# Performance work log

Measured on AMD Instinct MI355X. Metric: run time of the kernel, lower is better.

The kernel has to match this reference:

```python
import jax, jax.numpy as jnp
import numpy as np

N = 50000   # nodes
E = 800000  # edges
F = 256     # feature dim (in = hidden = out)
L = 3       # number_layers


def _arma_conv(x, src, dst, w, Wi, Wr, b):
    # GCN normalization without self loops (PyG ARMAConv default)
    deg = jax.ops.segment_sum(w, dst, num_segments=N)                 # [N]
    dinv = jnp.where(deg > 0, jax.lax.rsqrt(deg), 0.0)
    norm = dinv[src] * w * dinv[dst]                                   # [E]
    h = x @ Wi                                                         # [N, F]
    agg = jax.ops.segment_sum(norm[:, None] * h[src], dst, num_segments=N)  # [N, F]
    # root dropout is inactive in eval mode
    return jax.nn.relu(agg + x @ Wr + b)


def setup_inputs() -> dict:
    key = jax.random.key(0)
    ks = jax.random.split(key, 6)
    x = jax.random.normal(ks[0], (N, F), jnp.float32)
    edge_index = jax.random.randint(ks[1], (2, E), 0, N, jnp.int32)
    edge_attr = jax.random.uniform(ks[2], (E,), jnp.float32)
    s = 1.0 / np.sqrt(F)
    W_init = jax.random.normal(ks[3], (L, F, F), jnp.float32) * s
    W_root = jax.random.normal(ks[4], (L, F, F), jnp.float32) * s
    bias = jnp.zeros((L, F), jnp.float32)
    return dict(x=x, edge_index=edge_index, edge_attr=edge_attr,
                W_init=W_init, W_root=W_root, bias=bias)


def reference(x, edge_index, edge_attr, W_init, W_root, bias):
    src, dst = edge_index[0], edge_index[1]
    for i in range(L):  # fixed small layer count
        x = _arma_conv(x, src, dst, edge_attr, W_init[i], W_root[i], bias[i])
        # outer functional.relu is a no-op after the conv's internal ReLU;
        # dropout is inactive in eval mode.
    return x
```

## Files before the change

kernel.cpp:

```cpp
#include <hip/hip_runtime.h>
#include <hip/hip_bf16.h>

#define N_NODES 50000
#define N_EDGES 800000
#define FDIM 256
#define N_LAYERS 3
#define NB_SCAN ((N_NODES + 255) / 256)

typedef __attribute__((ext_vector_type(8))) short bf16x8;
typedef __attribute__((ext_vector_type(4))) float f32x4;

__device__ inline unsigned short f2bf(float f) {
  unsigned int u = __float_as_uint(f);
  unsigned int r = u + 0x7FFFu + ((u >> 16) & 1u);
  return (unsigned short)(r >> 16);
}
__device__ inline float bf2f(unsigned short s) {
  return __uint_as_float(((unsigned int)s) << 16);
}
__device__ inline void split2(float f, unsigned short& h, unsigned short& l) {
  h = f2bf(f);
  l = f2bf(f - bf2f(h));
}

#define GLOAD16(g, l) __builtin_amdgcn_global_load_lds( \
    (const __attribute__((address_space(1))) void*)(g), \
    (__attribute__((address_space(3))) void*)(l), 16, 0, 0)


__global__ void deg_count_kernel(const int* __restrict__ dst,
                                 const float* __restrict__ w,
                                 float* __restrict__ deg,
                                 int* __restrict__ cnt, int E) {
  int e = blockIdx.x * blockDim.x + threadIdx.x;
  if (e < E) {
    int d = dst[e];
    atomicAdd(&deg[d], w[e]);
    atomicAdd(&cnt[d], 1);
  }
}

__global__ void dinv_kernel(const float* __restrict__ deg,
                            float* __restrict__ dinv, int n) {
  int i = blockIdx.x * blockDim.x + threadIdx.x;
  if (i < n) {
    float d = deg[i];
    dinv[i] = (d > 0.f) ? (1.f / sqrtf(d)) : 0.f;
  }
}

__global__ __launch_bounds__(256)
void blocksum_kernel(const int* __restrict__ cnt, int* __restrict__ bsum, int n) {
  int b = blockIdx.x;
  int t = threadIdx.x;
  int i = b * 256 + t;
  int v = (i < n) ? cnt[i] : 0;
  #pragma unroll
  for (int d = 1; d < 64; d <<= 1) v += __shfl_xor(v, d, 64);
  __shared__ int ws[4];
  if ((t & 63) == 0) ws[t >> 6] = v;
  __syncthreads();
  if (t == 0) bsum[b] = ws[0] + ws[1] + ws[2] + ws[3];
}

__global__ __launch_bounds__(256)
void scanb_kernel(const int* __restrict__ bsum, int* __restrict__ bpre,
                  int* __restrict__ offs_end) {
  int t = threadIdx.x;
  int lane = t & 63, wid = t >> 6;
  int v = (t < NB_SCAN) ? bsum[t] : 0;
  int incl = v;
  #pragma unroll
  for (int d = 1; d < 64; d <<= 1) {
    int tmp = __shfl_up(incl, d, 64);
    if (lane >= d) incl += tmp;
  }
  __shared__ int wsum[4];
  if (lane == 63) wsum[wid] = incl;
  __syncthreads();
  if (t == 0) {
    int s = 0;
    #pragma unroll
    for (int k = 0; k < 4; ++k) { int tt = wsum[k]; wsum[k] = s; s += tt; }
  }
  __syncthreads();
  int excl = incl - v + wsum[wid];
  if (t < NB_SCAN) bpre[t] = excl;
  if (t == NB_SCAN - 1) *offs_end = excl + v;
}

__global__ __launch_bounds__(256)
void offs_kernel(const int* __restrict__ cnt, const int* __restrict__ bpre,
                 int* __restrict__ offs, int* __restrict__ cursor, int n) {
  int b = blockIdx.x;
  int t = threadIdx.x;
  int lane = t & 63, wid = t >> 6;
  int i = b * 256 + t;
  int v = (i < n) ? cnt[i] : 0;
  int incl = v;
  #pragma unroll
  for (int d = 1; d < 64; d <<= 1) {
    int tmp = __shfl_up(incl, d, 64);
    if (lane >= d) incl += tmp;
  }
  __shared__ int wsum[4];
  if (lane == 63) wsum[wid] = incl;
  __syncthreads();
  if (t == 0) {
    int s = 0;
    #pragma unroll
    for (int k = 0; k < 4; ++k) { int tt = wsum[k]; wsum[k] = s; s += tt; }
  }
  __syncthreads();
  int excl = incl - v + wsum[wid] + bpre[b];
  if (i < n) { offs[i] = excl; cursor[i] = excl; }
}

__global__ void scatter_kernel(const int* __restrict__ src,
                               const int* __restrict__ dst,
                               const float* __restrict__ w,
                               const float* __restrict__ dinv,
                               int* __restrict__ cursor,
                               int* __restrict__ src_s,
                               float* __restrict__ norm_s, int E) {
  int e = blockIdx.x * blockDim.x + threadIdx.x;
  if (e < E) {
    int s = src[e], d = dst[e];
    int pos = atomicAdd(&cursor[d], 1);
    src_s[pos] = s;
    norm_s[pos] = dinv[s] * w[e] * dinv[d];
  }
}

__global__ void split_kernel(const float* __restrict__ x,
                             unsigned short* __restrict__ xhi,
                             unsigned short* __restrict__ xlo, int n4) {
  int i = blockIdx.x * blockDim.x + threadIdx.x;
  if (i < n4) {
    float4 v = reinterpret_cast<const float4*>(x)[i];
    ushort4 h, l;
    split2(v.x, h.x, l.x);
    split2(v.y, h.y, l.y);
    split2(v.z, h.z, l.z);
    split2(v.w, h.w, l.w);
    reinterpret_cast<ushort4*>(xhi)[i] = h;
    reinterpret_cast<ushort4*>(xlo)[i] = l;
  }
}

__global__ __launch_bounds__(256)
void wsplit_kernel(const float* __restrict__ Wi_a,
                   const float* __restrict__ Wr_a,
                   unsigned short* __restrict__ wthi,
                   unsigned short* __restrict__ wtlo) {
  __shared__ float tile[32][33];
  int m6 = blockIdx.x >> 6;
  int tid = blockIdx.x & 63;
  int tk = (tid >> 3) * 32;
  int tn = (tid & 7) * 32;
  int layer = m6 >> 1;
  const float* W = ((m6 & 1) ? Wr_a : Wi_a) + (size_t)layer * FDIM * FDIM;
  int t = threadIdx.x;
  int lr = t >> 3;
  int lc = (t & 7) * 4;
  float4 v = *reinterpret_cast<const float4*>(W + (size_t)(tk + lr) * FDIM + tn + lc);
  tile[lr][lc + 0] = v.x; tile[lr][lc + 1] = v.y;
  tile[lr][lc + 2] = v.z; tile[lr][lc + 3] = v.w;
  __syncthreads();
  ushort4 h, l;
  split2(tile[lc + 0][lr], h.x, l.x);
  split2(tile[lc + 1][lr], h.y, l.y);
  split2(tile[lc + 2][lr], h.z, l.z);
  split2(tile[lc + 3][lr], h.w, l.w);
  size_t o = ((size_t)m6 * FDIM + tn + lr) * FDIM + tk + lc;
  *reinterpret_cast<ushort4*>(wthi + o) = h;
  *reinterpret_cast<ushort4*>(wtlo + o) = l;
}


__global__ __launch_bounds__(256)
void agg_kernel(const unsigned short* __restrict__ xh,
                const float* __restrict__ norm_s,
                const int* __restrict__ src_s,
                const int* __restrict__ offs,
                unsigned short* __restrict__ agh,
                unsigned short* __restrict__ agl, int n) {
  int node = blockIdx.x * 4 + (threadIdx.x >> 6);
  if (node >= n) return;
  int lane = threadIdx.x & 63;
  int beg = offs[node];
  int end = offs[node + 1];
  float a0 = 0.f, a1 = 0.f, a2 = 0.f, a3 = 0.f;
  int j = beg;
  for (; j + 4 <= end; j += 4) {
    int s0 = src_s[j], s1 = src_s[j + 1], s2 = src_s[j + 2], s3 = src_s[j + 3];
    float w0 = norm_s[j], w1 = norm_s[j + 1], w2 = norm_s[j + 2], w3 = norm_s[j + 3];
    ushort4 v0 = *reinterpret_cast<const ushort4*>(xh + (size_t)s0 * FDIM + lane * 4);
    ushort4 v1 = *reinterpret_cast<const ushort4*>(xh + (size_t)s1 * FDIM + lane * 4);
    ushort4 v2 = *reinterpret_cast<const ushort4*>(xh + (size_t)s2 * FDIM + lane * 4);
    ushort4 v3 = *reinterpret_cast<const ushort4*>(xh + (size_t)s3 * FDIM + lane * 4);
    a0 += w0 * bf2f(v0.x) + w1 * bf2f(v1.x) + w2 * bf2f(v2.x) + w3 * bf2f(v3.x);
    a1 += w0 * bf2f(v0.y) + w1 * bf2f(v1.y) + w2 * bf2f(v2.y) + w3 * bf2f(v3.y);
    a2 += w0 * bf2f(v0.z) + w1 * bf2f(v1.z) + w2 * bf2f(v2.z) + w3 * bf2f(v3.z);
    a3 += w0 * bf2f(v0.w) + w1 * bf2f(v1.w) + w2 * bf2f(v2.w) + w3 * bf2f(v3.w);
  }
  for (; j < end; ++j) {
    int s = src_s[j];
    float wv = norm_s[j];
    ushort4 v = *reinterpret_cast<const ushort4*>(xh + (size_t)s * FDIM + lane * 4);
    a0 += wv * bf2f(v.x); a1 += wv * bf2f(v.y);
    a2 += wv * bf2f(v.z); a3 += wv * bf2f(v.w);
  }
  ushort4 hh, ll;
  split2(a0, hh.x, ll.x);
  split2(a1, hh.y, ll.y);
  split2(a2, hh.z, ll.z);
  split2(a3, hh.w, ll.w);
  size_t base = (size_t)node * FDIM + lane * 4;
  *reinterpret_cast<ushort4*>(agh + base) = hh;
  *reinterpret_cast<ushort4*>(agl + base) = ll;
}


#define STAGE_TILE(TI, GPTR, ROWB, CLAMP, K0)                                     \
  {                                                                               \
    int s0_ = t;                                                                  \
    int rr_ = s0_ >> 2;                                                           \
    int sl_ = (s0_ & 3) ^ ((rr_ >> 1) & 3);                                       \
    int r2_ = (ROWB) + rr_; if (CLAMP && r2_ >= M) r2_ = M - 1;                   \
    GLOAD16((GPTR) + (size_t)r2_ * FDIM + (K0) + sl_ * 8,                         \
            smem + (TI) * 8192 + s0_ * 16);                                       \
    int s1_ = t + 256;                                                            \
    rr_ = s1_ >> 2;                                                               \
    sl_ = (s1_ & 3) ^ ((rr_ >> 1) & 3);                                           \
    r2_ = (ROWB) + rr_; if (CLAMP && r2_ >= M) r2_ = M - 1;                       \
    GLOAD16((GPTR) + (size_t)r2_ * FDIM + (K0) + sl_ * 8,                         \
            smem + (TI) * 8192 + s1_ * 16);                                       \
  }

#define STAGE_ALL(K0)                      \
  STAGE_TILE(0, agh, rowBase, 1, K0);      \
  STAGE_TILE(1, agl, rowBase, 1, K0);      \
  STAGE_TILE(2, xh, rowBase, 1, K0);       \
  STAGE_TILE(3, xl, rowBase, 1, K0);       \
  STAGE_TILE(4, wih, nBase, 0, K0);        \
  STAGE_TILE(5, wil, nBase, 0, K0);        \
  STAGE_TILE(6, wrh, nBase, 0, K0);        \
  STAGE_TILE(7, wrl, nBase, 0, K0);

__global__ __launch_bounds__(256, 2)
void gemm_dual_kernel(const unsigned short* __restrict__ agh,
                      const unsigned short* __restrict__ agl,
                      const unsigned short* __restrict__ xh,
                      const unsigned short* __restrict__ xl,
                      const unsigned short* __restrict__ wih,
                      const unsigned short* __restrict__ wil,
                      const unsigned short* __restrict__ wrh,
                      const unsigned short* __restrict__ wrl,
                      const float* __restrict__ bias,
                      unsigned short* __restrict__ oh,
                      unsigned short* __restrict__ ol,
                      float* __restrict__ ofinal,
                      int writeFinal, int M) {
  __shared__ __align__(16) unsigned char smem[65536];
  const int t = threadIdx.x;
  const int lane = t & 63;
  const int w = t >> 6;
  const int bid = blockIdx.x;
  const int rowBase = (bid >> 1) * 128;
  const int nBase = (bid & 1) * 128;

  const int wm = (w >> 1) * 64;
  const int wn = (w & 1) * 64;

  f32x4 acc[4][4];
  #pragma unroll
  for (int i = 0; i < 4; ++i)
    #pragma unroll
    for (int j = 0; j < 4; ++j)
      acc[i][j] = (f32x4)(0.f);

  STAGE_ALL(0);

  for (int s = 0; s < 8; ++s) {
    __syncthreads();

    const int q = lane >> 4;
    bf16x8 fah[4], fal[4], fxh[4], fxl[4];
    bf16x8 bih[4], bil[4], brh[4], brl[4];
    #pragma unroll
    for (int i = 0; i < 4; ++i) {
      int R = wm + i * 16 + (lane & 15);
      int offA = R * 64 + ((q ^ ((R >> 1) & 3)) * 16);
      fah[i] = *reinterpret_cast<const bf16x8*>(smem + offA);
      fal[i] = *reinterpret_cast<const bf16x8*>(smem + 8192 + offA);
      fxh[i] = *reinterpret_cast<const bf16x8*>(smem + 16384 + offA);
      fxl[i] = *reinterpret_cast<const bf16x8*>(smem + 24576 + offA);
      int Rb = wn + i * 16 + (lane & 15);
      int offB = Rb * 64 + ((q ^ ((Rb >> 1) & 3)) * 16);
      bih[i] = *reinterpret_cast<const bf16x8*>(smem + 32768 + offB);
      bil[i] = *reinterpret_cast<const bf16x8*>(smem + 40960 + offB);
      brh[i] = *reinterpret_cast<const bf16x8*>(smem + 49152 + offB);
      brl[i] = *reinterpret_cast<const bf16x8*>(smem + 57344 + offB);
    }
    asm volatile("s_waitcnt lgkmcnt(0)" ::: "memory");
    __builtin_amdgcn_sched_barrier(0);
    __builtin_amdgcn_s_barrier();
    __builtin_amdgcn_sched_barrier(0);

    if (s < 7) {
      int k1 = (s + 1) * 32;
      STAGE_ALL(k1);
    }

    #pragma unroll
    for (int j = 0; j < 4; ++j) {
      #pragma unroll
      for (int i = 0; i < 4; ++i) {
        acc[i][j] = __builtin_amdgcn_mfma_f32_16x16x32_bf16(fal[i], bih[j], acc[i][j], 0, 0, 0);
        acc[i][j] = __builtin_amdgcn_mfma_f32_16x16x32_bf16(fah[i], bil[j], acc[i][j], 0, 0, 0);
        acc[i][j] = __builtin_amdgcn_mfma_f32_16x16x32_bf16(fah[i], bih[j], acc[i][j], 0, 0, 0);
        acc[i][j] = __builtin_amdgcn_mfma_f32_16x16x32_bf16(fxl[i], brh[j], acc[i][j], 0, 0, 0);
        acc[i][j] = __builtin_amdgcn_mfma_f32_16x16x32_bf16(fxh[i], brl[j], acc[i][j], 0, 0, 0);
        acc[i][j] = __builtin_amdgcn_mfma_f32_16x16x32_bf16(fxh[i], brh[j], acc[i][j], 0, 0, 0);
      }
    }
  }

  const int cr = lane & 15;
  const int r4 = (lane >> 4) * 4;
  #pragma unroll
  for (int i = 0; i < 4; ++i)
    #pragma unroll
    for (int j = 0; j < 4; ++j) {
      int col = nBase + wn + j * 16 + cr;
      float badd = bias[col];
      #pragma unroll
      for (int e = 0; e < 4; ++e) {
        int row = rowBase + wm + i * 16 + r4 + e;
        if (row < M) {
          float val = fmaxf(acc[i][j][e] + badd, 0.f);
          size_t o = (size_t)row * FDIM + col;
          if (writeFinal) {
            ofinal[o] = val;
          } else {
            unsigned short hh, ll;
            split2(val, hh, ll);
            oh[o] = hh;
            ol[o] = ll;
          }
        }
      }
    }
}


extern "C" void kernel_launch(void* const* d_in, const int* in_sizes, int n_in,
                              void* d_out, int out_size, void* d_ws, size_t ws_size,
                              hipStream_t stream) {
  (void)in_sizes; (void)n_in; (void)out_size; (void)ws_size;
  const float* x0   = (const float*)d_in[0];
  const int*   ei   = (const int*)d_in[1];
  const float* ea   = (const float*)d_in[2];
  const float* Wi_a = (const float*)d_in[3];
  const float* Wr_a = (const float*)d_in[4];
  const float* b_a  = (const float*)d_in[5];
  float* out = (float*)d_out;

  const int* src = ei;
  const int* dst = ei + N_EDGES;

  char* ws = (char*)d_ws;
  size_t off = 0;
  auto alloc = [&](size_t bytes) {
    char* p = ws + off;
    off += (bytes + 255) & ~(size_t)255;
    return p;
  };
  const size_t NF2 = (size_t)N_NODES * FDIM * 2;
  unsigned short* XAh = (unsigned short*)alloc(NF2);
  unsigned short* XAl = (unsigned short*)alloc(NF2);
  unsigned short* XBh = (unsigned short*)alloc(NF2);
  unsigned short* XBl = (unsigned short*)alloc(NF2);
  unsigned short* agh = (unsigned short*)alloc(NF2);
  unsigned short* agl = (unsigned short*)alloc(NF2);
  unsigned short* wthi = (unsigned short*)alloc((size_t)N_LAYERS * 2 * FDIM * FDIM * 2);
  unsigned short* wtlo = (unsigned short*)alloc((size_t)N_LAYERS * 2 * FDIM * FDIM * 2);
  float* deg    = (float*)alloc((size_t)N_NODES * 4);
  float* dinv   = (float*)alloc((size_t)N_NODES * 4);
  int*   cnt    = (int*)alloc((size_t)N_NODES * 4);
  int*   offs   = (int*)alloc((size_t)(N_NODES + 1) * 4);
  int*   cursor = (int*)alloc((size_t)N_NODES * 4);
  int*   src_s  = (int*)alloc((size_t)N_EDGES * 4);
  float* norm_s = (float*)alloc((size_t)N_EDGES * 4);
  int*   bsum   = (int*)alloc((size_t)NB_SCAN * 4);
  int*   bpre   = (int*)alloc((size_t)NB_SCAN * 4);

  hipMemsetAsync(deg, 0, (size_t)N_NODES * 4, stream);
  hipMemsetAsync(cnt, 0, (size_t)N_NODES * 4, stream);

  deg_count_kernel<<<(N_EDGES + 255) / 256, 256, 0, stream>>>(dst, ea, deg, cnt, N_EDGES);
  dinv_kernel<<<(N_NODES + 255) / 256, 256, 0, stream>>>(deg, dinv, N_NODES);
  blocksum_kernel<<<NB_SCAN, 256, 0, stream>>>(cnt, bsum, N_NODES);
  scanb_kernel<<<1, 256, 0, stream>>>(bsum, bpre, offs + N_NODES);
  offs_kernel<<<NB_SCAN, 256, 0, stream>>>(cnt, bpre, offs, cursor, N_NODES);
  scatter_kernel<<<(N_EDGES + 255) / 256, 256, 0, stream>>>(src, dst, ea, dinv, cursor,
                                                            src_s, norm_s, N_EDGES);
  wsplit_kernel<<<6 * 64, 256, 0, stream>>>(Wi_a, Wr_a, wthi, wtlo);
  int n4 = N_NODES * FDIM / 4;
  split_kernel<<<(n4 + 255) / 256, 256, 0, stream>>>(x0, XAh, XAl, n4);

  const size_t WMAT = (size_t)FDIM * FDIM;
  int nrow = (N_NODES + 127) / 128;
  dim3 ggrid(nrow * 2);
  unsigned short* curh = XAh; unsigned short* curl = XAl;
  unsigned short* nxth = XBh; unsigned short* nxtl = XBl;
  for (int l = 0; l < N_LAYERS; ++l) {
    agg_kernel<<<(N_NODES + 3) / 4, 256, 0, stream>>>(curh, norm_s, src_s, offs,
                                                      agh, agl, N_NODES);
    int writeFinal = (l == N_LAYERS - 1) ? 1 : 0;
    gemm_dual_kernel<<<ggrid, 256, 0, stream>>>(
        agh, agl, curh, curl,
        wthi + (size_t)(l * 2) * WMAT, wtlo + (size_t)(l * 2) * WMAT,
        wthi + (size_t)(l * 2 + 1) * WMAT, wtlo + (size_t)(l * 2 + 1) * WMAT,
        b_a + (size_t)l * FDIM,
        nxth, nxtl, out, writeFinal, N_NODES);
    unsigned short* th = curh; unsigned short* tl = curl;
    curh = nxth; curl = nxtl; nxth = th; nxtl = tl;
  }
}
```

Before: 666.5 us.

## Double-buffer activation tiles in LDS, load weights from global, widen aggregation loads

The GEMM kernel now stages only the four activation tiles into LDS, double-buffered so the next k-slice loads while the current one is consumed. The weight fragments are read straight from global memory (cache-resident) instead of through LDS, which drops the second barrier per step. The aggregation kernel switches to half-wavefront-per-node with 16-byte gathers, so each wave covers two nodes. The trade-off is more global traffic for weights and possible latency stalls on those direct loads.

```diff
diff --git a/kernel.cpp b/kernel.cpp
--- a/kernel.cpp
+++ b/kernel.cpp
@@ -8,6 +8,7 @@
 #define NB_SCAN ((N_NODES + 255) / 256)
 
 typedef __attribute__((ext_vector_type(8))) short bf16x8;
+typedef __attribute__((ext_vector_type(8))) unsigned short u16x8;
 typedef __attribute__((ext_vector_type(4))) float f32x4;
 
 __device__ inline unsigned short f2bf(float f) {
@@ -185,68 +186,70 @@
                 const int* __restrict__ offs,
                 unsigned short* __restrict__ agh,
                 unsigned short* __restrict__ agl, int n) {
-  int node = blockIdx.x * 4 + (threadIdx.x >> 6);
+  int t = threadIdx.x;
+  int lane = t & 63;
+  int node = blockIdx.x * 8 + ((t >> 6) << 1) + (lane >> 5);
   if (node >= n) return;
-  int lane = threadIdx.x & 63;
+  int fl = lane & 31;
   int beg = offs[node];
   int end = offs[node + 1];
-  float a0 = 0.f, a1 = 0.f, a2 = 0.f, a3 = 0.f;
+  float a[8];
+  #pragma unroll
+  for (int f = 0; f < 8; ++f) a[f] = 0.f;
   int j = beg;
   for (; j + 4 <= end; j += 4) {
     int s0 = src_s[j], s1 = src_s[j + 1], s2 = src_s[j + 2], s3 = src_s[j + 3];
     float w0 = norm_s[j], w1 = norm_s[j + 1], w2 = norm_s[j + 2], w3 = norm_s[j + 3];
-    ushort4 v0 = *reinterpret_cast<const ushort4*>(xh + (size_t)s0 * FDIM + lane * 4);
-    ushort4 v1 = *reinterpret_cast<const ushort4*>(xh + (size_t)s1 * FDIM + lane * 4);
-    ushort4 v2 = *reinterpret_cast<const ushort4*>(xh + (size_t)s2 * FDIM + lane * 4);
-    ushort4 v3 = *reinterpret_cast<const ushort4*>(xh + (size_t)s3 * FDIM + lane * 4);
-    a0 += w0 * bf2f(v0.x) + w1 * bf2f(v1.x) + w2 * bf2f(v2.x) + w3 * bf2f(v3.x);
-    a1 += w0 * bf2f(v0.y) + w1 * bf2f(v1.y) + w2 * bf2f(v2.y) + w3 * bf2f(v3.y);
-    a2 += w0 * bf2f(v0.z) + w1 * bf2f(v1.z) + w2 * bf2f(v2.z) + w3 * bf2f(v3.z);
-    a3 += w0 * bf2f(v0.w) + w1 * bf2f(v1.w) + w2 * bf2f(v2.w) + w3 * bf2f(v3.w);
+    u16x8 v0 = *reinterpret_cast<const u16x8*>(xh + (size_t)s0 * FDIM + fl * 8);
+    u16x8 v1 = *reinterpret_cast<const u16x8*>(xh + (size_t)s1 * FDIM + fl * 8);
+    u16x8 v2 = *reinterpret_cast<const u16x8*>(xh + (size_t)s2 * FDIM + fl * 8);
+    u16x8 v3 = *reinterpret_cast<const u16x8*>(xh + (size_t)s3 * FDIM + fl * 8);
+    #pragma unroll
+    for (int f = 0; f < 8; ++f)
+      a[f] += w0 * bf2f(v0[f]) + w1 * bf2f(v1[f]) +
+              w2 * bf2f(v2[f]) + w3 * bf2f(v3[f]);
   }
   for (; j < end; ++j) {
     int s = src_s[j];
     float wv = norm_s[j];
-    ushort4 v = *reinterpret_cast<const ushort4*>(xh + (size_t)s * FDIM + lane * 4);
-    a0 += wv * bf2f(v.x); a1 += wv * bf2f(v.y);
-    a2 += wv * bf2f(v.z); a3 += wv * bf2f(v.w);
-  }
-  ushort4 hh, ll;
-  split2(a0, hh.x, ll.x);
-  split2(a1, hh.y, ll.y);
-  split2(a2, hh.z, ll.z);
-  split2(a3, hh.w, ll.w);
-  size_t base = (size_t)node * FDIM + lane * 4;
-  *reinterpret_cast<ushort4*>(agh + base) = hh;
-  *reinterpret_cast<ushort4*>(agl + base) = ll;
-}
-
-
-#define STAGE_TILE(TI, GPTR, ROWB, CLAMP, K0)                                     \
+    u16x8 v = *reinterpret_cast<const u16x8*>(xh + (size_t)s * FDIM + fl * 8);
+    #pragma unroll
+    for (int f = 0; f < 8; ++f) a[f] += wv * bf2f(v[f]);
+  }
+  u16x8 hh, ll;
+  #pragma unroll
+  for (int f = 0; f < 8; ++f) {
+    unsigned short h, l;
+    split2(a[f], h, l);
+    hh[f] = h; ll[f] = l;
+  }
+  size_t base = (size_t)node * FDIM + fl * 8;
+  *reinterpret_cast<u16x8*>(agh + base) = hh;
+  *reinterpret_cast<u16x8*>(agl + base) = ll;
+}
+
+
+#define STAGE_TILE(BASE, TI, GPTR, K0)                                            \
   {                                                                               \
     int s0_ = t;                                                                  \
     int rr_ = s0_ >> 2;                                                           \
     int sl_ = (s0_ & 3) ^ ((rr_ >> 1) & 3);                                       \
-    int r2_ = (ROWB) + rr_; if (CLAMP && r2_ >= M) r2_ = M - 1;                   \
+    int r2_ = rowBase + rr_; if (r2_ >= M) r2_ = M - 1;                           \
     GLOAD16((GPTR) + (size_t)r2_ * FDIM + (K0) + sl_ * 8,                         \
-            smem + (TI) * 8192 + s0_ * 16);                                       \
+            (BASE) + (TI) * 8192 + s0_ * 16);                                     \
     int s1_ = t + 256;                                                            \
     rr_ = s1_ >> 2;                                                               \
     sl_ = (s1_ & 3) ^ ((rr_ >> 1) & 3);                                           \
-    r2_ = (ROWB) + rr_; if (CLAMP && r2_ >= M) r2_ = M - 1;                       \
+    r2_ = rowBase + rr_; if (r2_ >= M) r2_ = M - 1;                               \
     GLOAD16((GPTR) + (size_t)r2_ * FDIM + (K0) + sl_ * 8,                         \
-            smem + (TI) * 8192 + s1_ * 16);                                       \
-  }
-
-#define STAGE_ALL(K0)                      \
-  STAGE_TILE(0, agh, rowBase, 1, K0);      \
-  STAGE_TILE(1, agl, rowBase, 1, K0);      \
-  STAGE_TILE(2, xh, rowBase, 1, K0);       \
-  STAGE_TILE(3, xl, rowBase, 1, K0);       \
-  STAGE_TILE(4, wih, nBase, 0, K0);        \
-  STAGE_TILE(5, wil, nBase, 0, K0);        \
-  STAGE_TILE(6, wrh, nBase, 0, K0);        \
-  STAGE_TILE(7, wrl, nBase, 0, K0);
+            (BASE) + (TI) * 8192 + s1_ * 16);                                     \
+  }
+
+#define STAGE_A(BASE, K0)                  \
+  STAGE_TILE(BASE, 0, agh, K0);            \
+  STAGE_TILE(BASE, 1, agl, K0);            \
+  STAGE_TILE(BASE, 2, xh, K0);             \
+  STAGE_TILE(BASE, 3, xl, K0);
 
 __global__ __launch_bounds__(256, 2)
 void gemm_dual_kernel(const unsigned short* __restrict__ agh,
@@ -272,6 +275,7 @@
 
   const int wm = (w >> 1) * 64;
   const int wn = (w & 1) * 64;
+  const int q = lane >> 4;
 
   f32x4 acc[4][4];
   #pragma unroll
@@ -280,49 +284,45 @@
     for (int j = 0; j < 4; ++j)
       acc[i][j] = (f32x4)(0.f);
 
-  STAGE_ALL(0);
+  STAGE_A(smem, 0);
 
   for (int s = 0; s < 8; ++s) {
     __syncthreads();
-
-    const int q = lane >> 4;
-    bf16x8 fah[4], fal[4], fxh[4], fxl[4];
-    bf16x8 bih[4], bil[4], brh[4], brl[4];
+    unsigned char* cur = smem + (s & 1) * 32768;
+    unsigned char* nxt = smem + ((s + 1) & 1) * 32768;
+    const int k0 = s * 32;
+
+    bf16x8 Bih[4], Bil[4], Brh[4], Brl[4];
+    #pragma unroll
+    for (int j = 0; j < 4; ++j) {
+      size_t bo = (size_t)(nBase + wn + j * 16 + (lane & 15)) * FDIM + k0 + q * 8;
+      Bih[j] = *reinterpret_cast<const bf16x8*>(wih + bo);
+      Bil[j] = *reinterpret_cast<const bf16x8*>(wil + bo);
+      Brh[j] = *reinterpret_cast<const bf16x8*>(wrh + bo);
+      Brl[j] = *reinterpret_cast<const bf16x8*>(wrl + bo);
+    }
+    __builtin_amdgcn_sched_barrier(0);
+
+    if (s < 7) {
+      STAGE_A(nxt, k0 + 32);
+    }
+
     #pragma unroll
     for (int i = 0; i < 4; ++i) {
       int R = wm + i * 16 + (lane & 15);
       int offA = R * 64 + ((q ^ ((R >> 1) & 3)) * 16);
-      fah[i] = *reinterpret_cast<const bf16x8*>(smem + offA);
-      fal[i] = *reinterpret_cast<const bf16x8*>(smem + 8192 + offA);
-      fxh[i] = *reinterpret_cast<const bf16x8*>(smem + 16384 + offA);
-      fxl[i] = *reinterpret_cast<const bf16x8*>(smem + 24576 + offA);
-      int Rb = wn + i * 16 + (lane & 15);
-      int offB = Rb * 64 + ((q ^ ((Rb >> 1) & 3)) * 16);
-      bih[i] = *reinterpret_cast<const bf16x8*>(smem + 32768 + offB);
-      bil[i] = *reinterpret_cast<const bf16x8*>(smem + 40960 + offB);
-      brh[i] = *reinterpret_cast<const bf16x8*>(smem + 49152 + offB);
-      brl[i] = *reinterpret_cast<const bf16x8*>(smem + 57344 + offB);
-    }
-    asm volatile("s_waitcnt lgkmcnt(0)" ::: "memory");
-    __builtin_amdgcn_sched_barrier(0);
-    __builtin_amdgcn_s_barrier();
-    __builtin_amdgcn_sched_barrier(0);
-
-    if (s < 7) {
-      int k1 = (s + 1) * 32;
-      STAGE_ALL(k1);
-    }
-
-    #pragma unroll
-    for (int j = 0; j < 4; ++j) {
+      bf16x8 fah = *reinterpret_cast<const bf16x8*>(cur + offA);
+      bf16x8 fal = *reinterpret_cast<const bf16x8*>(cur + 8192 + offA);
+      bf16x8 fxh = *reinterpret_cast<const bf16x8*>(cur + 16384 + offA);
+      bf16x8 fxl = *reinterpret_cast<const bf16x8*>(cur + 24576 + offA);
       #pragma unroll
-      for (int i = 0; i < 4; ++i) {
-        acc[i][j] = __builtin_amdgcn_mfma_f32_16x16x32_bf16(fal[i], bih[j], acc[i][j], 0, 0, 0);
-        acc[i][j] = __builtin_amdgcn_mfma_f32_16x16x32_bf16(fah[i], bil[j], acc[i][j], 0, 0, 0);
-        acc[i][j] = __builtin_amdgcn_mfma_f32_16x16x32_bf16(fah[i], bih[j], acc[i][j], 0, 0, 0);
-        acc[i][j] = __builtin_amdgcn_mfma_f32_16x16x32_bf16(fxl[i], brh[j], acc[i][j], 0, 0, 0);
-        acc[i][j] = __builtin_amdgcn_mfma_f32_16x16x32_bf16(fxh[i], brl[j], acc[i][j], 0, 0, 0);
-        acc[i][j] = __builtin_amdgcn_mfma_f32_16x16x32_bf16(fxh[i], brh[j], acc[i][j], 0, 0, 0);
+      for (int j = 0; j < 4; ++j) {
+        acc[i][j] = __builtin_amdgcn_mfma_f32_16x16x32_bf16(fal, Bih[j], acc[i][j], 0, 0, 0);
+        acc[i][j] = __builtin_amdgcn_mfma_f32_16x16x32_bf16(fah, Bil[j], acc[i][j], 0, 0, 0);
+        acc[i][j] = __builtin_amdgcn_mfma_f32_16x16x32_bf16(fah, Bih[j], acc[i][j], 0, 0, 0);
+        acc[i][j] = __builtin_amdgcn_mfma_f32_16x16x32_bf16(fxl, Brh[j], acc[i][j], 0, 0, 0);
+        acc[i][j] = __builtin_amdgcn_mfma_f32_16x16x32_bf16(fxh, Brl[j], acc[i][j], 0, 0, 0);
+        acc[i][j] = __builtin_amdgcn_mfma_f32_16x16x32_bf16(fxh, Brh[j], acc[i][j], 0, 0, 0);
       }
     }
   }
@@ -416,7 +416,7 @@
   unsigned short* curh = XAh; unsigned short* curl = XAl;
   unsigned short* nxth = XBh; unsigned short* nxtl = XBl;
   for (int l = 0; l < N_LAYERS; ++l) {
-    agg_kernel<<<(N_NODES + 3) / 4, 256, 0, stream>>>(curh, norm_s, src_s, offs,
+    agg_kernel<<<(N_NODES + 7) / 8, 256, 0, stream>>>(curh, norm_s, src_s, offs,
                                                       agh, agl, N_NODES);
     int writeFinal = (l == N_LAYERS - 1) ? 1 : 0;
     gemm_dual_kernel<<<ggrid, 256, 0, stream>>>(
```

Measured after the change: 758.9 us. 13.9% more time.

## Widen aggregation gathers to 16-byte loads and remap GEMM blocks per XCD

Applied to the files above, without the earlier changes.

The aggregation kernel now gives each node 32 lanes that each load 8 bf16 features per 16-byte load, instead of 64 lanes loading 4. It also unrolls the edge loop by 8, so more gathers are in flight per wave. Separately, the dual GEMM remaps block IDs so that consecutive tiles, which share the same row block of A and X, land on the same XCD for better L2 reuse. The trade-off is higher register pressure in the aggregation kernel and a more complex block-index mapping.

```diff
diff --git a/kernel.cpp b/kernel.cpp
--- a/kernel.cpp
+++ b/kernel.cpp
@@ -8,6 +8,7 @@
 #define NB_SCAN ((N_NODES + 255) / 256)
 
 typedef __attribute__((ext_vector_type(8))) short bf16x8;
+typedef __attribute__((ext_vector_type(8))) unsigned short u16x8;
 typedef __attribute__((ext_vector_type(4))) float f32x4;
 
 __device__ inline unsigned short f2bf(float f) {
@@ -185,40 +186,50 @@
                 const int* __restrict__ offs,
                 unsigned short* __restrict__ agh,
                 unsigned short* __restrict__ agl, int n) {
-  int node = blockIdx.x * 4 + (threadIdx.x >> 6);
+  int t = threadIdx.x;
+  int lane = t & 63;
+  int node = blockIdx.x * 8 + ((t >> 6) << 1) + (lane >> 5);
   if (node >= n) return;
-  int lane = threadIdx.x & 63;
+  int fl = lane & 31;
   int beg = offs[node];
   int end = offs[node + 1];
-  float a0 = 0.f, a1 = 0.f, a2 = 0.f, a3 = 0.f;
+  float a[8];
+  #pragma unroll
+  for (int f = 0; f < 8; ++f) a[f] = 0.f;
+  const unsigned short* xbase = xh + fl * 8;
   int j = beg;
-  for (; j + 4 <= end; j += 4) {
-    int s0 = src_s[j], s1 = src_s[j + 1], s2 = src_s[j + 2], s3 = src_s[j + 3];
-    float w0 = norm_s[j], w1 = norm_s[j + 1], w2 = norm_s[j + 2], w3 = norm_s[j + 3];
-    ushort4 v0 = *reinterpret_cast<const ushort4*>(xh + (size_t)s0 * FDIM + lane * 4);
-    ushort4 v1 = *reinterpret_cast<const ushort4*>(xh + (size_t)s1 * FDIM + lane * 4);
-    ushort4 v2 = *reinterpret_cast<const ushort4*>(xh + (size_t)s2 * FDIM + lane * 4);
-    ushort4 v3 = *reinterpret_cast<const ushort4*>(xh + (size_t)s3 * FDIM + lane * 4);
-    a0 += w0 * bf2f(v0.x) + w1 * bf2f(v1.x) + w2 * bf2f(v2.x) + w3 * bf2f(v3.x);
-    a1 += w0 * bf2f(v0.y) + w1 * bf2f(v1.y) + w2 * bf2f(v2.y) + w3 * bf2f(v3.y);
-    a2 += w0 * bf2f(v0.z) + w1 * bf2f(v1.z) + w2 * bf2f(v2.z) + w3 * bf2f(v3.z);
-    a3 += w0 * bf2f(v0.w) + w1 * bf2f(v1.w) + w2 * bf2f(v2.w) + w3 * bf2f(v3.w);
+  for (; j + 8 <= end; j += 8) {
+    int sj[8];
+    float wj[8];
+    #pragma unroll
+    for (int u = 0; u < 8; ++u) { sj[u] = src_s[j + u]; wj[u] = norm_s[j + u]; }
+    u16x8 v[8];
+    #pragma unroll
+    for (int u = 0; u < 8; ++u)
+      v[u] = *reinterpret_cast<const u16x8*>(xbase + (size_t)sj[u] * FDIM);
+    #pragma unroll
+    for (int u = 0; u < 8; ++u)
+      #pragma unroll
+      for (int f = 0; f < 8; ++f)
+        a[f] += wj[u] * bf2f(v[u][f]);
   }
   for (; j < end; ++j) {
     int s = src_s[j];
     float wv = norm_s[j];
-    ushort4 v = *reinterpret_cast<const ushort4*>(xh + (size_t)s * FDIM + lane * 4);
-    a0 += wv * bf2f(v.x); a1 += wv * bf2f(v.y);
-    a2 += wv * bf2f(v.z); a3 += wv * bf2f(v.w);
-  }
-  ushort4 hh, ll;
-  split2(a0, hh.x, ll.x);
-  split2(a1, hh.y, ll.y);
-  split2(a2, hh.z, ll.z);
-  split2(a3, hh.w, ll.w);
-  size_t base = (size_t)node * FDIM + lane * 4;
-  *reinterpret_cast<ushort4*>(agh + base) = hh;
-  *reinterpret_cast<ushort4*>(agl + base) = ll;
+    u16x8 v = *reinterpret_cast<const u16x8*>(xbase + (size_t)s * FDIM);
+    #pragma unroll
+    for (int f = 0; f < 8; ++f) a[f] += wv * bf2f(v[f]);
+  }
+  u16x8 hh, ll;
+  #pragma unroll
+  for (int f = 0; f < 8; ++f) {
+    unsigned short h, l;
+    split2(a[f], h, l);
+    hh[f] = h; ll[f] = l;
+  }
+  size_t base = (size_t)node * FDIM + fl * 8;
+  *reinterpret_cast<u16x8*>(agh + base) = hh;
+  *reinterpret_cast<u16x8*>(agl + base) = ll;
 }
 
 
@@ -266,9 +277,14 @@
   const int t = threadIdx.x;
   const int lane = t & 63;
   const int w = t >> 6;
-  const int bid = blockIdx.x;
-  const int rowBase = (bid >> 1) * 128;
-  const int nBase = (bid & 1) * 128;
+
+  const int nwg = gridDim.x;
+  const int bq = nwg >> 3, br = nwg & 7;
+  const int xcd = blockIdx.x & 7;
+  const int idx = blockIdx.x >> 3;
+  const int wgid = (xcd < br ? xcd * (bq + 1) : br * (bq + 1) + (xcd - br) * bq) + idx;
+  const int rowBase = (wgid >> 1) * 128;
+  const int nBase = (wgid & 1) * 128;
 
   const int wm = (w >> 1) * 64;
   const int wn = (w & 1) * 64;
@@ -416,7 +432,7 @@
   unsigned short* curh = XAh; unsigned short* curl = XAl;
   unsigned short* nxth = XBh; unsigned short* nxtl = XBl;
   for (int l = 0; l < N_LAYERS; ++l) {
-    agg_kernel<<<(N_NODES + 3) / 4, 256, 0, stream>>>(curh, norm_s, src_s, offs,
+    agg_kernel<<<(N_NODES + 7) / 8, 256, 0, stream>>>(curh, norm_s, src_s, offs,
                                                       agh, agl, N_NODES);
     int writeFinal = (l == N_LAYERS - 1) ? 1 : 0;
     gemm_dual_kernel<<<ggrid, 256, 0, stream>>>(
```

After: 627.9 us. 5.8% less time.
